# Performance work log

Hardware: AMD Instinct MI355X
Metric: run time of the kernel (lower is better)

## Reference

```python
import jax, jax.numpy as jnp
import numpy as np

NUM_K_HEADS = 16
NUM_V_HEADS = 32
HEAD_K = 64
HEAD_V = 64
KERNEL = 4
KEY_DIM = NUM_K_HEADS * HEAD_K      # 1024
VAL_DIM = NUM_V_HEADS * HEAD_V      # 2048
CONV_DIM = 2 * KEY_DIM + VAL_DIM    # 4096
T = 2048


def setup_inputs() -> dict:
    key = jax.random.key(0)
    ks = jax.random.split(key, 6)
    return {
        "mixed_qkv": jax.random.normal(ks[0], (T, CONV_DIM), jnp.float32),
        "conv_state_in": jnp.zeros((1, KERNEL - 1, CONV_DIM), jnp.float32),
        "recurrent_state_in": jnp.zeros((1, NUM_V_HEADS, HEAD_K, HEAD_V), jnp.float32),
        "b": jax.random.normal(ks[1], (T, NUM_V_HEADS), jnp.float32),
        "a": jax.random.normal(ks[2], (T, NUM_V_HEADS), jnp.float32),
        "conv1d_weight": jax.random.normal(ks[3], (CONV_DIM, KERNEL), jnp.float32) * 0.1,
        "A_log": jax.random.normal(ks[4], (NUM_V_HEADS,), jnp.float32) * 0.1,
        "dt_bias": jax.random.normal(ks[5], (NUM_V_HEADS,), jnp.float32) * 0.1,
    }


def _causal_conv1d_prefill(x, weight, init_state):
    """Depthwise causal conv1d with silu. x:[T,D], weight:[D,W], init_state:[W-1,D]."""
    W = weight.shape[1]
    t = x.shape[0]
    padded = jnp.concatenate([init_state, x], axis=0)  # [T+W-1, D]
    out = padded[0:t] * weight[:, 0]
    for w in range(1, W):  # tiny fixed-width loop (W=4), fused by XLA
        out = out + padded[w:w + t] * weight[:, w]
    return jax.nn.silu(out)


def _l2norm(x, eps=1e-6):
    return x * jax.lax.rsqrt(jnp.sum(x * x, axis=-1, keepdims=True) + eps)


def reference(mixed_qkv, conv_state_in, recurrent_state_in, b, a, conv1d_weight, A_log, dt_bias):
    # --- causal conv over the prefill sequence (batch slice [:1] as in the module) ---
    conv_out = _causal_conv1d_prefill(mixed_qkv, conv1d_weight, conv_state_in[0])  # [T, CONV_DIM]
    t = conv_out.shape[0]

    # --- split into q/k/v heads ---
    q = conv_out[:, :KEY_DIM].reshape(t, NUM_K_HEADS, HEAD_K)
    k = conv_out[:, KEY_DIM:2 * KEY_DIM].reshape(t, NUM_K_HEADS, HEAD_K)
    v = conv_out[:, 2 * KEY_DIM:].reshape(t, NUM_V_HEADS, HEAD_V)
    rep = NUM_V_HEADS // NUM_K_HEADS
    if rep > 1:
        q = jnp.repeat(q, rep, axis=1)
        k = jnp.repeat(k, rep, axis=1)

    # --- gates ---
    beta = jax.nn.sigmoid(b.astype(jnp.float32))                       # [T, H]
    g = -jnp.exp(A_log)[None] * jax.nn.softplus(a.astype(jnp.float32) + dt_bias[None])  # [T, H]

    # --- qk l2-norm and scale (use_qk_l2norm=True) ---
    qn = _l2norm(q) * (HEAD_K ** -0.5)
    kn = _l2norm(k)

    # --- gated delta-rule recurrence over time ---
    def step(S, inp):
        q_t, k_t, v_t, g_t, b_t = inp  # [H,dk],[H,dk],[H,dv],[H],[H]
        S = S * jnp.exp(g_t)[:, None, None]                      # decay
        kv = jnp.einsum('hkv,hk->hv', S, k_t)                    # memory read
        u = b_t[:, None] * (v_t - kv)                            # delta update
        S = S + jnp.einsum('hk,hv->hkv', k_t, u)
        o = jnp.einsum('hkv,hk->hv', S, q_t)
        return S, o

    S0 = recurrent_state_in[0]  # [H, dk, dv]
    _, core_attn_out = jax.lax.scan(step, S0, (qn, kn, v, g, beta))
    return core_attn_out  # [T, H_v, head_v_dim]
```

## Files before the change

kernel.cpp:

```cpp
#include <hip/hip_runtime.h>
#include <math.h>

#define T_LEN   2048
#define NKH     16
#define NVH     32
#define HD      64
#define KEY_DIM 1024
#define VAL_DIM 2048
#define CONV_DIM 4096
#define NCHUNK  32
#define CL      64

typedef float fl4 __attribute__((ext_vector_type(4)));

__device__ __forceinline__ float sigmoid_f(float x) { return 1.f / (1.f + __expf(-x)); }
__device__ __forceinline__ float rdlane(float v, int i) {
    return __int_as_float(__builtin_amdgcn_readlane(__float_as_int(v), i));
}

__global__ __launch_bounds__(256) void prep_kernel(
    const float* __restrict__ x,
    const float* __restrict__ cs,
    const float* __restrict__ w,
    const float* __restrict__ bsrc,
    const float* __restrict__ a,
    const float* __restrict__ A_log,
    const float* __restrict__ dt_bias,
    float* __restrict__ qn,
    float* __restrict__ kn,
    float* __restrict__ vb,
    float* __restrict__ g,
    float* __restrict__ beta)
{
    const int t   = blockIdx.x;
    const int tid = threadIdx.x;
    const int d0  = tid * 16;

    fl4 r4[4];
    #pragma unroll
    for (int grp = 0; grp < 4; ++grp) {
        const int d = d0 + grp * 4;
        fl4 xv[4], wq[4];
        #pragma unroll
        for (int wi = 0; wi < 4; ++wi) {
            const int row = t - 3 + wi;
            const float* src = (row >= 0) ? (x + (size_t)row * CONV_DIM + d)
                                          : (cs + (size_t)(row + 3) * CONV_DIM + d);
            xv[wi] = *(const fl4*)src;
        }
        #pragma unroll
        for (int j = 0; j < 4; ++j) wq[j] = *(const fl4*)(w + (size_t)(d + j) * 4);
        #pragma unroll
        for (int j = 0; j < 4; ++j) {
            float acc = xv[0][j] * wq[j][0];
            acc = fmaf(xv[1][j], wq[j][1], acc);
            acc = fmaf(xv[2][j], wq[j][2], acc);
            acc = fmaf(xv[3][j], wq[j][3], acc);
            r4[grp][j] = acc * sigmoid_f(acc);
        }
    }

    if (tid < 128) {
        float ss = 0.f;
        #pragma unroll
        for (int grp = 0; grp < 4; ++grp)
            #pragma unroll
            for (int j = 0; j < 4; ++j) ss = fmaf(r4[grp][j], r4[grp][j], ss);
        ss += __shfl_xor(ss, 1);
        ss += __shfl_xor(ss, 2);
        const bool is_q = (tid < 64);
        float scale = (is_q ? 0.125f : 1.0f) / sqrtf(ss + 1e-6f);
        float* dst = is_q ? (qn + (size_t)t * KEY_DIM + d0)
                          : (kn + (size_t)t * KEY_DIM + (d0 - KEY_DIM));
        #pragma unroll
        for (int grp = 0; grp < 4; ++grp) {
            fl4 o;
            #pragma unroll
            for (int j = 0; j < 4; ++j) o[j] = r4[grp][j] * scale;
            *(fl4*)(dst + grp * 4) = o;
        }
    } else {
        const int hh = (d0 - 2 * KEY_DIM) >> 6;
        const float bb = sigmoid_f(bsrc[(size_t)t * NVH + hh]);
        float* dst = vb + (size_t)t * VAL_DIM + (d0 - 2 * KEY_DIM);
        #pragma unroll
        for (int grp = 0; grp < 4; ++grp) {
            fl4 o;
            #pragma unroll
            for (int j = 0; j < 4; ++j) o[j] = r4[grp][j] * bb;
            *(fl4*)(dst + grp * 4) = o;
        }
    }

    if (tid < 32) {
        float av = a[(size_t)t * NVH + tid] + dt_bias[tid];
        float sp = fmaxf(av, 0.f) + log1pf(__expf(-fabsf(av)));
        g[(size_t)t * NVH + tid]    = -__expf(A_log[tid]) * sp;
        beta[(size_t)t * NVH + tid] = sigmoid_f(bsrc[(size_t)t * NVH + tid]);
    }
}

__global__ __launch_bounds__(256) void phase1_kernel(
    const float* __restrict__ qn, const float* __restrict__ kn,
    const float* __restrict__ gws, const float* __restrict__ bws,
    float* __restrict__ gam_g, float* __restrict__ bg_g,
    float* __restrict__ KT_g, float* __restrict__ QT_g,
    float* __restrict__ MTt_g, float* __restrict__ SUt_g)
{
    const int bid = blockIdx.x;
    const int c = bid >> 5, h = bid & 31, kh = h >> 1;
    const int tid = threadIdx.x, lane = tid & 63, wv = tid >> 6;

    __shared__ float Ks[64][68], Qs[64][68], Am[64][68], Tm[64][68];
    __shared__ float Gs[64], Dend[64], Bet[64];
    __shared__ float Xs[4][16][17];

    #pragma unroll
    for (int p = 0; p < 4; ++p) {
        int idx = p * 256 + tid;
        int t = idx >> 4, i4 = (idx & 15) * 4;
        *(fl4*)&Ks[t][i4] = *(const fl4*)&kn[(size_t)(c*64+t)*KEY_DIM + kh*64 + i4];
        *(fl4*)&Qs[t][i4] = *(const fl4*)&qn[(size_t)(c*64+t)*KEY_DIM + kh*64 + i4];
    }
    for (int idx = tid; idx < 64*64; idx += 256) {
        int t = idx >> 6, s = idx & 63;
        Tm[t][s] = (t == s) ? 1.f : 0.f;
    }
    if (tid < 64) {
        float gv = gws[(size_t)(c*64+lane)*NVH + h];
        #pragma unroll
        for (int d = 1; d < 64; d <<= 1) {
            float nv = __shfl_up(gv, d);
            if (lane >= d) gv += nv;
        }
        Gs[lane] = gv;
        float g63 = __shfl(gv, 63);
        Dend[lane] = __expf(g63 - gv);
        float bb = bws[(size_t)(c*64+lane)*NVH + h];
        Bet[lane] = bb;
        float ga = __expf(gv);
        gam_g[(size_t)(c*NVH+h)*64 + lane] = ga;
        bg_g[(size_t)(c*NVH+h)*64 + lane]  = ga * bb;
    }
    __syncthreads();

    if ((h & 1) == 0) {
        float* kdst = KT_g + (size_t)(c*NKH + kh)*64*64;
        float* qdst = QT_g + (size_t)(c*NKH + kh)*64*64;
        const int t = lane;
        #pragma unroll
        for (int ii = 0; ii < 16; ++ii) {
            int i = wv*16 + ii;
            kdst[i*64 + t] = Ks[t][i];
            qdst[i*64 + t] = Qs[t][i];
        }
    }

    float accK[16], accQ[16];
    {
        #pragma unroll
        for (int j = 0; j < 16; ++j) { accK[j] = 0.f; accQ[j] = 0.f; }
        const int t = lane, sbase = wv * 16;
        for (int i4 = 0; i4 < 64; i4 += 4) {
            fl4 kt = *(const fl4*)&Ks[t][i4];
            fl4 qt = *(const fl4*)&Qs[t][i4];
            #pragma unroll
            for (int sj = 0; sj < 16; ++sj) {
                fl4 ks = *(const fl4*)&Ks[sbase + sj][i4];
                accK[sj] += kt[0]*ks[0] + kt[1]*ks[1] + kt[2]*ks[2] + kt[3]*ks[3];
                accQ[sj] += qt[0]*ks[0] + qt[1]*ks[1] + qt[2]*ks[2] + qt[3]*ks[3];
            }
        }
    }
    __syncthreads();
    {
        const int t = lane, sbase = wv * 16;
        const float gt = Gs[t], bt = Bet[t];
        #pragma unroll
        for (int sj = 0; sj < 16; ++sj) {
            int s = sbase + sj;
            float e = __expf(gt - Gs[s]);
            Am[t][s] = (s < t)  ? bt * e * accK[sj] : 0.f;
            Qs[t][s] = (s <= t) ? e * accQ[sj] : 0.f;
        }
    }
    __syncthreads();

    if (lane < 16) {
        const int base = wv * 16;
        const int sj = lane, s = base + sj;
        for (int tl = 1; tl < 16; ++tl) {
            int t = base + tl;
            if (sj < tl) {
                float acc = 0.f;
                for (int il = sj; il < tl; ++il)
                    acc += Am[t][base + il] * Tm[base + il][s];
                Tm[t][s] = -acc;
            }
        }
    }
    for (int L = 1; L <= 3; ++L) {
        __syncthreads();
        if (wv < 4 - L) {
            const int J = wv, I = wv + L;
            const int r = lane & 15, cg = lane >> 4;
            float X[4] = {0.f,0.f,0.f,0.f};
            for (int Kb = J; Kb < I; ++Kb) {
                #pragma unroll
                for (int p = 0; p < 16; ++p) {
                    float av = Am[I*16 + r][Kb*16 + p];
                    #pragma unroll
                    for (int mm = 0; mm < 4; ++mm)
                        X[mm] += av * Tm[Kb*16 + p][J*16 + cg + 4*mm];
                }
            }
            #pragma unroll
            for (int mm = 0; mm < 4; ++mm) Xs[wv][r][cg + 4*mm] = X[mm];
            float Y[4] = {0.f,0.f,0.f,0.f};
            #pragma unroll
            for (int p = 0; p < 16; ++p) {
                float td = Tm[I*16 + r][I*16 + p];
                #pragma unroll
                for (int mm = 0; mm < 4; ++mm)
                    Y[mm] += td * Xs[wv][p][cg + 4*mm];
            }
            #pragma unroll
            for (int mm = 0; mm < 4; ++mm)
                Tm[I*16 + r][J*16 + cg + 4*mm] = -Y[mm];
        }
    }
    __syncthreads();

    {
        float acc[16];
        #pragma unroll
        for (int j = 0; j < 16; ++j) acc[j] = 0.f;
        const int t = lane, sbase = wv * 16;
        for (int i4 = 0; i4 < 64; i4 += 4) {
            fl4 mv = *(const fl4*)&Qs[t][i4];
            #pragma unroll
            for (int sj = 0; sj < 16; ++sj) {
                int s = sbase + sj;
                acc[sj] += mv[0]*Tm[i4+0][s] + mv[1]*Tm[i4+1][s]
                         + mv[2]*Tm[i4+2][s] + mv[3]*Tm[i4+3][s];
            }
        }
        float* dst = MTt_g + (size_t)(c*NVH + h)*64*64;
        #pragma unroll
        for (int sj = 0; sj < 16; ++sj)
            dst[(sbase + sj)*64 + t] = acc[sj];
    }
    {
        float acc[16];
        #pragma unroll
        for (int j = 0; j < 16; ++j) acc[j] = 0.f;
        const int d = lane, sbase = wv * 16;
        for (int t = 0; t < 64; ++t) {
            float kd = Ks[t][d] * Dend[t];
            #pragma unroll
            for (int sj = 0; sj < 16; ++sj)
                acc[sj] += kd * Tm[t][sbase + sj];
        }
        float* dst = SUt_g + (size_t)(c*NVH + h)*64*64;
        #pragma unroll
        for (int sj = 0; sj < 16; ++sj)
            dst[(sbase + sj)*64 + d] = acc[sj];
    }
}

__global__ __launch_bounds__(256) void phase2_kernel(
    const float* __restrict__ vbp, const float* __restrict__ gam_g,
    const float* __restrict__ bg_g, const float* __restrict__ KT_g,
    const float* __restrict__ QT_g, const float* __restrict__ MTt_g,
    const float* __restrict__ SUt_g, const float* __restrict__ rs0,
    float* __restrict__ out)
{
    const int bid = blockIdx.x;
    const int h = bid & 31, jg = bid >> 5, kh = h >> 1;
    const int tid = threadIdx.x, lane = tid & 63, wv = tid >> 6;
    const int mv = wv >> 1;
    const int jb = (wv & 1) * 4;

    __shared__ float bufA[8192];
    __shared__ float bufB[8192];
    __shared__ float s0s[64][12], wshs[64][12], o1s[64][12];

    {
        int idx = tid * 2;
        int d = idx >> 3, j = idx & 7;
        s0s[d][j]     = rs0[((size_t)h*64 + d)*64 + jg*8 + j];
        s0s[d][j + 1] = rs0[((size_t)h*64 + d)*64 + jg*8 + j + 1];
    }

    const int base = wv * 1024 + lane * 4;

    fl4 rA0, rA1, rA2, rA3, rA4, rA5, rA6, rA7;
    {
        const float* kt = KT_g + (size_t)kh * 4096 + base;
        const float* qt = QT_g + (size_t)kh * 4096 + base;
        rA0 = *(const fl4*)(kt);       rA1 = *(const fl4*)(kt + 256);
        rA2 = *(const fl4*)(kt + 512); rA3 = *(const fl4*)(kt + 768);
        rA4 = *(const fl4*)(qt);       rA5 = *(const fl4*)(qt + 256);
        rA6 = *(const fl4*)(qt + 512); rA7 = *(const fl4*)(qt + 768);
    }

    for (int c = 0; c < NCHUNK; ++c) {
        *(fl4*)&bufA[base      ] = rA0; *(fl4*)&bufA[base +  256] = rA1;
        *(fl4*)&bufA[base +  512] = rA2; *(fl4*)&bufA[base +  768] = rA3;
        *(fl4*)&bufA[4096 + base      ] = rA4; *(fl4*)&bufA[4096 + base +  256] = rA5;
        *(fl4*)&bufA[4096 + base +  512] = rA6; *(fl4*)&bufA[4096 + base +  768] = rA7;

        fl4 rB0, rB1, rB2, rB3, rB4, rB5, rB6, rB7;
        {
            const float* mt = MTt_g + (size_t)(c*NVH + h)*4096 + base;
            const float* su = SUt_g + (size_t)(c*NVH + h)*4096 + base;
            rB0 = *(const fl4*)(mt);       rB1 = *(const fl4*)(mt + 256);
            rB2 = *(const fl4*)(mt + 512); rB3 = *(const fl4*)(mt + 768);
            rB4 = *(const fl4*)(su);       rB5 = *(const fl4*)(su + 256);
            rB6 = *(const fl4*)(su + 512); rB7 = *(const fl4*)(su + 768);
        }

        const float* gamc = gam_g + (size_t)(c*NVH + h)*64;
        const float* bgc  = bg_g  + (size_t)(c*NVH + h)*64;
        const float gend = gamc[63];
        fl4 vbv = {0.f, 0.f, 0.f, 0.f};
        float bgl = 0.f, gml = 0.f;
        if (mv == 0) {
            vbv = *(const fl4*)&vbp[(size_t)(c*64 + lane)*VAL_DIM + h*64 + jg*8 + jb];
            bgl = bgc[lane];
        } else {
            gml = gamc[lane];
        }

        __syncthreads();

        fl4 sa = *(const fl4*)&s0s[lane][jb];
        float a0 = 0.f, a1 = 0.f, a2 = 0.f, a3 = 0.f;
        {
            const float* mb = &bufA[mv * 4096 + lane];
            #pragma unroll
            for (int i = 0; i < 64; ++i) {
                float m = mb[i * 64];
                a0 = fmaf(m, rdlane(sa[0], i), a0);
                a1 = fmaf(m, rdlane(sa[1], i), a1);
                a2 = fmaf(m, rdlane(sa[2], i), a2);
                a3 = fmaf(m, rdlane(sa[3], i), a3);
            }
        }
        if (mv == 0) {
            fl4 wv4;
            wv4[0] = vbv[0] - bgl * a0; wv4[1] = vbv[1] - bgl * a1;
            wv4[2] = vbv[2] - bgl * a2; wv4[3] = vbv[3] - bgl * a3;
            *(fl4*)&wshs[lane][jb] = wv4;
        } else {
            fl4 o4;
            o4[0] = gml * a0; o4[1] = gml * a1; o4[2] = gml * a2; o4[3] = gml * a3;
            *(fl4*)&o1s[lane][jb] = o4;
        }
        __syncthreads();

        *(fl4*)&bufB[base      ] = rB0; *(fl4*)&bufB[base +  256] = rB1;
        *(fl4*)&bufB[base +  512] = rB2; *(fl4*)&bufB[base +  768] = rB3;
        *(fl4*)&bufB[4096 + base      ] = rB4; *(fl4*)&bufB[4096 + base +  256] = rB5;
        *(fl4*)&bufB[4096 + base +  512] = rB6; *(fl4*)&bufB[4096 + base +  768] = rB7;

        if (c + 1 < NCHUNK) {
            const float* kt = KT_g + (size_t)((c+1)*NKH + kh)*4096 + base;
            const float* qt = QT_g + (size_t)((c+1)*NKH + kh)*4096 + base;
            rA0 = *(const fl4*)(kt);       rA1 = *(const fl4*)(kt + 256);
            rA2 = *(const fl4*)(kt + 512); rA3 = *(const fl4*)(kt + 768);
            rA4 = *(const fl4*)(qt);       rA5 = *(const fl4*)(qt + 256);
            rA6 = *(const fl4*)(qt + 512); rA7 = *(const fl4*)(qt + 768);
        }
        __syncthreads();

        fl4 sb = *(const fl4*)&wshs[lane][jb];
        float b0 = 0.f, b1 = 0.f, b2 = 0.f, b3 = 0.f;
        {
            const float* mb = &bufB[mv * 4096 + lane];
            #pragma unroll
            for (int i = 0; i < 64; ++i) {
                float m = mb[i * 64];
                b0 = fmaf(m, rdlane(sb[0], i), b0);
                b1 = fmaf(m, rdlane(sb[1], i), b1);
                b2 = fmaf(m, rdlane(sb[2], i), b2);
                b3 = fmaf(m, rdlane(sb[3], i), b3);
            }
        }
        if (mv == 0) {
            fl4 o1v = *(const fl4*)&o1s[lane][jb];
            fl4 ov;
            ov[0] = o1v[0] + b0; ov[1] = o1v[1] + b1;
            ov[2] = o1v[2] + b2; ov[3] = o1v[3] + b3;
            *(fl4*)&out[(size_t)(c*64 + lane)*VAL_DIM + h*64 + jg*8 + jb] = ov;
        } else {
            fl4 sv = *(const fl4*)&s0s[lane][jb];
            fl4 nv;
            nv[0] = gend * sv[0] + b0; nv[1] = gend * sv[1] + b1;
            nv[2] = gend * sv[2] + b2; nv[3] = gend * sv[3] + b3;
            *(fl4*)&s0s[lane][jb] = nv;
        }
        __syncthreads();
    }
}

#define LOADSTEP(KA, QA, VV, GG, BB, tt) {                                     \
    _Pragma("unroll")                                                          \
    for (int i = 0; i < 4; ++i) {                                              \
        KA[i] = *(const fl4*)(kp + (size_t)(tt) * KEY_DIM + i * 4);            \
        QA[i] = *(const fl4*)(qp + (size_t)(tt) * KEY_DIM + i * 4);            \
    }                                                                          \
    VV = vp[(size_t)(tt) * VAL_DIM];                                           \
    GG = gp[(size_t)(tt) * NVH];                                               \
    BB = bp[(size_t)(tt) * NVH];                                               \
}

#define COMPUTE(KA, QA, VV, GG, BB, tt) {                                      \
    const float dec = __expf(GG);                                              \
    float c0 = 0.f, c1 = 0.f, c2 = 0.f, c3 = 0.f;                              \
    _Pragma("unroll")                                                          \
    for (int i = 0; i < 4; ++i) {                                              \
        S[i*4+0] *= dec; S[i*4+1] *= dec; S[i*4+2] *= dec; S[i*4+3] *= dec;    \
        c0 = fmaf(S[i*4+0], KA[i][0], c0);                                     \
        c1 = fmaf(S[i*4+1], KA[i][1], c1);                                     \
        c2 = fmaf(S[i*4+2], KA[i][2], c2);                                     \
        c3 = fmaf(S[i*4+3], KA[i][3], c3);                                     \
    }                                                                          \
    float kv = (c0 + c1) + (c2 + c3);                                          \
    kv += __shfl_xor(kv, 1);                                                   \
    kv += __shfl_xor(kv, 2);                                                   \
    const float u = VV - BB * kv;                                              \
    float o0 = 0.f, o1 = 0.f, o2 = 0.f, o3 = 0.f;                              \
    _Pragma("unroll")                                                          \
    for (int i = 0; i < 4; ++i) {                                              \
        S[i*4+0] = fmaf(KA[i][0], u, S[i*4+0]);                                \
        S[i*4+1] = fmaf(KA[i][1], u, S[i*4+1]);                                \
        S[i*4+2] = fmaf(KA[i][2], u, S[i*4+2]);                                \
        S[i*4+3] = fmaf(KA[i][3], u, S[i*4+3]);                                \
        o0 = fmaf(S[i*4+0], QA[i][0], o0);                                     \
        o1 = fmaf(S[i*4+1], QA[i][1], o1);                                     \
        o2 = fmaf(S[i*4+2], QA[i][2], o2);                                     \
        o3 = fmaf(S[i*4+3], QA[i][3], o3);                                     \
    }                                                                          \
    float oo = (o0 + o1) + (o2 + o3);                                          \
    oo += __shfl_xor(oo, 1);                                                   \
    oo += __shfl_xor(oo, 2);                                                   \
    if (kg == 0) op[(size_t)(tt) * VAL_DIM] = oo;                              \
}

__global__ __launch_bounds__(256) void scan_kernel(
    const float* __restrict__ qn, const float* __restrict__ kn,
    const float* __restrict__ v, const float* __restrict__ g,
    const float* __restrict__ bet, const float* __restrict__ rs0,
    float* __restrict__ out)
{
    const int h    = blockIdx.x;
    const int kh   = h >> 1;
    const int tid  = threadIdx.x;
    const int vcol = tid >> 2;
    const int kg   = tid & 3;

    float S[16];
    #pragma unroll
    for (int j = 0; j < 16; ++j)
        S[j] = rs0[((size_t)h * HD + (kg * 16 + j)) * HD + vcol];

    const float* kp = kn + (size_t)kh * HD + kg * 16;
    const float* qp = qn + (size_t)kh * HD + kg * 16;
    const float* vp = v + (size_t)h * HD + vcol;
    const float* gp = g + h;
    const float* bp = bet + h;
    float*       op = out + (size_t)h * HD + vcol;

    fl4 ka0[4], qa0[4]; float vv0, gg0, bb0;
    fl4 ka1[4], qa1[4]; float vv1, gg1, bb1;

    LOADSTEP(ka0, qa0, vv0, gg0, bb0, 0);
    for (int t = 0; t < T_LEN; t += 2) {
        LOADSTEP(ka1, qa1, vv1, gg1, bb1, t + 1);
        COMPUTE(ka0, qa0, vv0, gg0, bb0, t);
        const int t2 = (t + 2 < T_LEN) ? (t + 2) : (T_LEN - 1);
        LOADSTEP(ka0, qa0, vv0, gg0, bb0, t2);
        COMPUTE(ka1, qa1, vv1, gg1, bb1, t + 1);
    }
}

extern "C" void kernel_launch(void* const* d_in, const int* in_sizes, int n_in,
                              void* d_out, int out_size, void* d_ws, size_t ws_size,
                              hipStream_t stream)
{
    const float* x       = (const float*)d_in[0];
    const float* cs      = (const float*)d_in[1];
    const float* rs0     = (const float*)d_in[2];
    const float* b       = (const float*)d_in[3];
    const float* a       = (const float*)d_in[4];
    const float* w       = (const float*)d_in[5];
    const float* A_log   = (const float*)d_in[6];
    const float* dt_bias = (const float*)d_in[7];
    float* out = (float*)d_out;

    float* ws = (float*)d_ws;
    size_t off = 0;
    float* qn  = ws + off; off += (size_t)T_LEN * KEY_DIM;
    float* kn  = ws + off; off += (size_t)T_LEN * KEY_DIM;
    float* vb  = ws + off; off += (size_t)T_LEN * VAL_DIM;
    float* g   = ws + off; off += (size_t)T_LEN * NVH;
    float* be  = ws + off; off += (size_t)T_LEN * NVH;
    float* gam = ws + off; off += (size_t)NCHUNK * NVH * 64;
    float* bg  = ws + off; off += (size_t)NCHUNK * NVH * 64;
    float* KT  = ws + off; off += (size_t)NCHUNK * NKH * 64 * 64;
    float* QT  = ws + off; off += (size_t)NCHUNK * NKH * 64 * 64;
    float* MTt = ws + off; off += (size_t)NCHUNK * NVH * 64 * 64;
    float* SUt = ws + off; off += (size_t)NCHUNK * NVH * 64 * 64;
    const size_t need = off * sizeof(float);

    prep_kernel<<<T_LEN, 256, 0, stream>>>(x, cs, w, b, a, A_log, dt_bias,
                                           qn, kn, vb, g, be);
    if (ws_size >= need) {
        phase1_kernel<<<NCHUNK * NVH, 256, 0, stream>>>(qn, kn, g, be,
                                                        gam, bg, KT, QT, MTt, SUt);
        phase2_kernel<<<NVH * 8, 256, 0, stream>>>(vb, gam, bg, KT, QT, MTt, SUt,
                                                   rs0, out);
    } else {
        scan_kernel<<<NVH, 256, 0, stream>>>(qn, kn, vb, g, be, rs0, out);
    }
}
```

Measured before the change: 304.2 us.

## Split phase2 value columns across more blocks and vectorize phase1 Tm reads

Phase2 now gives each block 4 value columns instead of 8, doubling the grid from 256 to 512 blocks so more compute units work on the serial chunk recurrence. Each block does half the FMA work per chunk but still loads the full K/Q/M/S matrices, so global and LDS traffic per output column doubles. Phase1's two small matmuls now read Tm rows as float4 vectors with explicit fmaf instead of scalar strided loads, to cut LDS instruction count.

After: 304.5 us. Within noise of the previous version (+0.1%).

```diff
diff --git a/kernel.cpp b/kernel.cpp
--- a/kernel.cpp
+++ b/kernel.cpp
@@ -236,13 +236,21 @@
         #pragma unroll
         for (int j = 0; j < 16; ++j) acc[j] = 0.f;
         const int t = lane, sbase = wv * 16;
-        for (int i4 = 0; i4 < 64; i4 += 4) {
-            fl4 mv = *(const fl4*)&Qs[t][i4];
-            #pragma unroll
-            for (int sj = 0; sj < 16; ++sj) {
-                int s = sbase + sj;
-                acc[sj] += mv[0]*Tm[i4+0][s] + mv[1]*Tm[i4+1][s]
-                         + mv[2]*Tm[i4+2][s] + mv[3]*Tm[i4+3][s];
+        for (int i = 0; i < 64; i += 4) {
+            fl4 mv4 = *(const fl4*)&Qs[t][i];
+            #pragma unroll
+            for (int r = 0; r < 4; ++r) {
+                fl4 ta = *(const fl4*)&Tm[i+r][sbase + 0];
+                fl4 tb = *(const fl4*)&Tm[i+r][sbase + 4];
+                fl4 tc = *(const fl4*)&Tm[i+r][sbase + 8];
+                fl4 td = *(const fl4*)&Tm[i+r][sbase + 12];
+                #pragma unroll
+                for (int q = 0; q < 4; ++q) {
+                    acc[q]      = fmaf(mv4[r], ta[q], acc[q]);
+                    acc[4 + q]  = fmaf(mv4[r], tb[q], acc[4 + q]);
+                    acc[8 + q]  = fmaf(mv4[r], tc[q], acc[8 + q]);
+                    acc[12 + q] = fmaf(mv4[r], td[q], acc[12 + q]);
+                }
             }
         }
         float* dst = MTt_g + (size_t)(c*NVH + h)*64*64;
@@ -257,9 +265,17 @@
         const int d = lane, sbase = wv * 16;
         for (int t = 0; t < 64; ++t) {
             float kd = Ks[t][d] * Dend[t];
-            #pragma unroll
-            for (int sj = 0; sj < 16; ++sj)
-                acc[sj] += kd * Tm[t][sbase + sj];
+            fl4 ta = *(const fl4*)&Tm[t][sbase + 0];
+            fl4 tb = *(const fl4*)&Tm[t][sbase + 4];
+            fl4 tc = *(const fl4*)&Tm[t][sbase + 8];
+            fl4 td = *(const fl4*)&Tm[t][sbase + 12];
+            #pragma unroll
+            for (int q = 0; q < 4; ++q) {
+                acc[q]      = fmaf(kd, ta[q], acc[q]);
+                acc[4 + q]  = fmaf(kd, tb[q], acc[4 + q]);
+                acc[8 + q]  = fmaf(kd, tc[q], acc[8 + q]);
+                acc[12 + q] = fmaf(kd, td[q], acc[12 + q]);
+            }
         }
         float* dst = SUt_g + (size_t)(c*NVH + h)*64*64;
         #pragma unroll
@@ -279,54 +295,52 @@
     const int h = bid & 31, jg = bid >> 5, kh = h >> 1;
     const int tid = threadIdx.x, lane = tid & 63, wv = tid >> 6;
     const int mv = wv >> 1;
-    const int jb = (wv & 1) * 4;
+    const int jb = (wv & 1) * 2;
 
     __shared__ float bufA[8192];
     __shared__ float bufB[8192];
-    __shared__ float s0s[64][12], wshs[64][12], o1s[64][12];
+    __shared__ float s0s[64][6], wshs[64][6], o1s[64][6];
 
     {
-        int idx = tid * 2;
-        int d = idx >> 3, j = idx & 7;
-        s0s[d][j]     = rs0[((size_t)h*64 + d)*64 + jg*8 + j];
-        s0s[d][j + 1] = rs0[((size_t)h*64 + d)*64 + jg*8 + j + 1];
-    }
-
-    const int base = wv * 1024 + lane * 4;
+        int d = tid >> 2, j = tid & 3;
+        s0s[d][j] = rs0[((size_t)h*64 + d)*64 + jg*4 + j];
+    }
+
+    const int base = tid * 4;
 
     fl4 rA0, rA1, rA2, rA3, rA4, rA5, rA6, rA7;
     {
         const float* kt = KT_g + (size_t)kh * 4096 + base;
         const float* qt = QT_g + (size_t)kh * 4096 + base;
-        rA0 = *(const fl4*)(kt);       rA1 = *(const fl4*)(kt + 256);
-        rA2 = *(const fl4*)(kt + 512); rA3 = *(const fl4*)(kt + 768);
-        rA4 = *(const fl4*)(qt);       rA5 = *(const fl4*)(qt + 256);
-        rA6 = *(const fl4*)(qt + 512); rA7 = *(const fl4*)(qt + 768);
+        rA0 = *(const fl4*)(kt);        rA1 = *(const fl4*)(kt + 1024);
+        rA2 = *(const fl4*)(kt + 2048); rA3 = *(const fl4*)(kt + 3072);
+        rA4 = *(const fl4*)(qt);        rA5 = *(const fl4*)(qt + 1024);
+        rA6 = *(const fl4*)(qt + 2048); rA7 = *(const fl4*)(qt + 3072);
     }
 
     for (int c = 0; c < NCHUNK; ++c) {
-        *(fl4*)&bufA[base      ] = rA0; *(fl4*)&bufA[base +  256] = rA1;
-        *(fl4*)&bufA[base +  512] = rA2; *(fl4*)&bufA[base +  768] = rA3;
-        *(fl4*)&bufA[4096 + base      ] = rA4; *(fl4*)&bufA[4096 + base +  256] = rA5;
-        *(fl4*)&bufA[4096 + base +  512] = rA6; *(fl4*)&bufA[4096 + base +  768] = rA7;
+        *(fl4*)&bufA[base       ] = rA0; *(fl4*)&bufA[base + 1024] = rA1;
+        *(fl4*)&bufA[base + 2048] = rA2; *(fl4*)&bufA[base + 3072] = rA3;
+        *(fl4*)&bufA[base + 4096] = rA4; *(fl4*)&bufA[base + 5120] = rA5;
+        *(fl4*)&bufA[base + 6144] = rA6; *(fl4*)&bufA[base + 7168] = rA7;
 
         fl4 rB0, rB1, rB2, rB3, rB4, rB5, rB6, rB7;
         {
             const float* mt = MTt_g + (size_t)(c*NVH + h)*4096 + base;
             const float* su = SUt_g + (size_t)(c*NVH + h)*4096 + base;
-            rB0 = *(const fl4*)(mt);       rB1 = *(const fl4*)(mt + 256);
-            rB2 = *(const fl4*)(mt + 512); rB3 = *(const fl4*)(mt + 768);
-            rB4 = *(const fl4*)(su);       rB5 = *(const fl4*)(su + 256);
-            rB6 = *(const fl4*)(su + 512); rB7 = *(const fl4*)(su + 768);
+            rB0 = *(const fl4*)(mt);        rB1 = *(const fl4*)(mt + 1024);
+            rB2 = *(const fl4*)(mt + 2048); rB3 = *(const fl4*)(mt + 3072);
+            rB4 = *(const fl4*)(su);        rB5 = *(const fl4*)(su + 1024);
+            rB6 = *(const fl4*)(su + 2048); rB7 = *(const fl4*)(su + 3072);
         }
 
         const float* gamc = gam_g + (size_t)(c*NVH + h)*64;
         const float* bgc  = bg_g  + (size_t)(c*NVH + h)*64;
         const float gend = gamc[63];
-        fl4 vbv = {0.f, 0.f, 0.f, 0.f};
-        float bgl = 0.f, gml = 0.f;
+        float vb0 = 0.f, vb1 = 0.f, bgl = 0.f, gml = 0.f;
         if (mv == 0) {
-            vbv = *(const fl4*)&vbp[(size_t)(c*64 + lane)*VAL_DIM + h*64 + jg*8 + jb];
+            const float* vp = &vbp[(size_t)(c*64 + lane)*VAL_DIM + h*64 + jg*4 + jb];
+            vb0 = vp[0]; vb1 = vp[1];
             bgl = bgc[lane];
         } else {
             gml = gamc[lane];
@@ -334,71 +348,59 @@
 
         __syncthreads();
 
-        fl4 sa = *(const fl4*)&s0s[lane][jb];
-        float a0 = 0.f, a1 = 0.f, a2 = 0.f, a3 = 0.f;
+        float sa0 = s0s[lane][jb], sa1 = s0s[lane][jb + 1];
+        float a0 = 0.f, a1 = 0.f;
         {
             const float* mb = &bufA[mv * 4096 + lane];
             #pragma unroll
             for (int i = 0; i < 64; ++i) {
                 float m = mb[i * 64];
-                a0 = fmaf(m, rdlane(sa[0], i), a0);
-                a1 = fmaf(m, rdlane(sa[1], i), a1);
-                a2 = fmaf(m, rdlane(sa[2], i), a2);
-                a3 = fmaf(m, rdlane(sa[3], i), a3);
+                a0 = fmaf(m, rdlane(sa0, i), a0);
+                a1 = fmaf(m, rdlane(sa1, i), a1);
             }
         }
         if (mv == 0) {
-            fl4 wv4;
-            wv4[0] = vbv[0] - bgl * a0; wv4[1] = vbv[1] - bgl * a1;
-            wv4[2] = vbv[2] - bgl * a2; wv4[3] = vbv[3] - bgl * a3;
-            *(fl4*)&wshs[lane][jb] = wv4;
+            wshs[lane][jb]     = vb0 - bgl * a0;
+            wshs[lane][jb + 1] = vb1 - bgl * a1;
         } else {
-            fl4 o4;
-            o4[0] = gml * a0; o4[1] = gml * a1; o4[2] = gml * a2; o4[3] = gml * a3;
-            *(fl4*)&o1s[lane][jb] = o4;
+            o1s[lane][jb]     = gml * a0;
+            o1s[lane][jb + 1] = gml * a1;
         }
         __syncthreads();
 
-        *(fl4*)&bufB[base      ] = rB0; *(fl4*)&bufB[base +  256] = rB1;
-        *(fl4*)&bufB[base +  512] = rB2; *(fl4*)&bufB[base +  768] = rB3;
-        *(fl4*)&bufB[4096 + base      ] = rB4; *(fl4*)&bufB[4096 + base +  256] = rB5;
-        *(fl4*)&bufB[4096 + base +  512] = rB6; *(fl4*)&bufB[4096 + base +  768] = rB7;
+        *(fl4*)&bufB[base       ] = rB0; *(fl4*)&bufB[base + 1024] = rB1;
+        *(fl4*)&bufB[base + 2048] = rB2; *(fl4*)&bufB[base + 3072] = rB3;
+        *(fl4*)&bufB[base + 4096] = rB4; *(fl4*)&bufB[base + 5120] = rB5;
+        *(fl4*)&bufB[base + 6144] = rB6; *(fl4*)&bufB[base + 7168] = rB7;
 
         if (c + 1 < NCHUNK) {
             const float* kt = KT_g + (size_t)((c+1)*NKH + kh)*4096 + base;
             const float* qt = QT_g + (size_t)((c+1)*NKH + kh)*4096 + base;
-            rA0 = *(const fl4*)(kt);       rA1 = *(const fl4*)(kt + 256);
-            rA2 = *(const fl4*)(kt + 512); rA3 = *(const fl4*)(kt + 768);
-            rA4 = *(const fl4*)(qt);       rA5 = *(const fl4*)(qt + 256);
-            rA6 = *(const fl4*)(qt + 512); rA7 = *(const fl4*)(qt + 768);
+            rA0 = *(const fl4*)(kt);        rA1 = *(const fl4*)(kt + 1024);
+            rA2 = *(const fl4*)(kt + 2048); rA3 = *(const fl4*)(kt + 3072);
+            rA4 = *(const fl4*)(qt);        rA5 = *(const fl4*)(qt + 1024);
+            rA6 = *(const fl4*)(qt + 2048); rA7 = *(const fl4*)(qt + 3072);
         }
         __syncthreads();
 
-        fl4 sb = *(const fl4*)&wshs[lane][jb];
-        float b0 = 0.f, b1 = 0.f, b2 = 0.f, b3 = 0.f;
+        float sb0 = wshs[lane][jb], sb1 = wshs[lane][jb + 1];
+        float b0 = 0.f, b1 = 0.f;
         {
             const float* mb = &bufB[mv * 4096 + lane];
             #pragma unroll
             for (int i = 0; i < 64; ++i) {
                 float m = mb[i * 64];
-                b0 = fmaf(m, rdlane(sb[0], i), b0);
-                b1 = fmaf(m, rdlane(sb[1], i), b1);
-                b2 = fmaf(m, rdlane(sb[2], i), b2);
-                b3 = fmaf(m, rdlane(sb[3], i), b3);
+                b0 = fmaf(m, rdlane(sb0, i), b0);
+                b1 = fmaf(m, rdlane(sb1, i), b1);
             }
         }
         if (mv == 0) {
-            fl4 o1v = *(const fl4*)&o1s[lane][jb];
-            fl4 ov;
-            ov[0] = o1v[0] + b0; ov[1] = o1v[1] + b1;
-            ov[2] = o1v[2] + b2; ov[3] = o1v[3] + b3;
-            *(fl4*)&out[(size_t)(c*64 + lane)*VAL_DIM + h*64 + jg*8 + jb] = ov;
+            float* op = &out[(size_t)(c*64 + lane)*VAL_DIM + h*64 + jg*4 + jb];
+            op[0] = o1s[lane][jb]     + b0;
+            op[1] = o1s[lane][jb + 1] + b1;
         } else {
-            fl4 sv = *(const fl4*)&s0s[lane][jb];
-            fl4 nv;
-            nv[0] = gend * sv[0] + b0; nv[1] = gend * sv[1] + b1;
-            nv[2] = gend * sv[2] + b2; nv[3] = gend * sv[3] + b3;
-            *(fl4*)&s0s[lane][jb] = nv;
+            s0s[lane][jb]     = gend * s0s[lane][jb]     + b0;
+            s0s[lane][jb + 1] = gend * s0s[lane][jb + 1] + b1;
         }
         __syncthreads();
     }
@@ -519,8 +521,8 @@
     if (ws_size >= need) {
         phase1_kernel<<<NCHUNK * NVH, 256, 0, stream>>>(qn, kn, g, be,
                                                         gam, bg, KT, QT, MTt, SUt);
-        phase2_kernel<<<NVH * 8, 256, 0, stream>>>(vb, gam, bg, KT, QT, MTt, SUt,
-                                                   rs0, out);
+        phase2_kernel<<<NVH * 16, 256, 0, stream>>>(vb, gam, bg, KT, QT, MTt, SUt,
+                                                    rs0, out);
     } else {
         scan_kernel<<<NVH, 256, 0, stream>>>(qn, kn, vb, g, be, rs0, out);
     }
```
